# Kernel tuning notes

Measured on AMD Instinct MI355X. Metric: run time of the kernel, lower is better.

## Reference

```python
import jax, jax.numpy as jnp
import numpy as np

B, L, D, O = 16, 128, 256, 256

def setup_inputs() -> dict:
    key = jax.random.key(0)
    k1, k2, k3, k4, k5 = jax.random.split(key, 5)
    text = jax.random.normal(k1, (B, L, D), dtype=jnp.float32)
    adj = jax.random.uniform(k2, (B, L, L), dtype=jnp.float32)
    dep_embed = jax.random.normal(k3, (B, L, L, D), dtype=jnp.float32)
    weight = jax.random.normal(k4, (D, O), dtype=jnp.float32) * (1.0 / np.sqrt(D))
    bias = jax.random.normal(k5, (O,), dtype=jnp.float32) * 0.01
    return {"text": text, "adj": adj, "dep_embed": dep_embed, "weight": weight, "bias": bias}

def reference(text, adj, dep_embed, weight, bias):
    # val_sum[b,j,i,d] = text[b,j,d] + dep_embed[b,j,i,d]
    val_sum = text[:, :, None, :] + dep_embed            # [B,L,L,D]
    hidden = val_sum @ weight                            # [B,L,L,O]
    # torch: output[b,i,o] = sum_j adj[b,i,j] * hidden[b,j,i,o]
    out = jnp.einsum('bij,bjio->bio', adj, hidden)       # [B,L,O]
    out = out + bias
    return jax.nn.relu(out)
```

## Files before the change

### kernel.cpp

```cpp
#include <hip/hip_runtime.h>


constexpr int Bc = 16, Lc = 128, Dc = 256, Oc = 256;
constexpr int ITILE = 4;

__global__ __launch_bounds__(256)
void gc_fused(const float4* __restrict__ text4,
              const float*  __restrict__ adj,
              const float4* __restrict__ dep4,
              const float4* __restrict__ weight4,
              const float4* __restrict__ bias4,
              float4* __restrict__ out4)
{
    const int b  = blockIdx.x >> 5;
    const int i0 = (blockIdx.x & 31) * ITILE;
    const int t  = threadIdx.x;
    const int ig = t >> 6;
    const int dg = t & 63;

    __shared__ float s_adj[ITILE][Lc];
    __shared__ float s_S[ITILE][Dc];

    for (int k = t; k < ITILE * Lc; k += 256) {
        int row = k >> 7;
        int col = k & (Lc - 1);
        s_adj[row][col] = adj[((b * Lc) + i0 + row) * Lc + col];
    }
    __syncthreads();

    const int i = i0 + ig;

    float4 acc = {0.f, 0.f, 0.f, 0.f};
    const float4* tb = text4 + (size_t)b * Lc * (Dc / 4) + dg;
    const float4* db = dep4  + ((size_t)b * Lc * Lc + (size_t)i) * (Dc / 4) + dg;
    #pragma unroll 4
    for (int j = 0; j < Lc; ++j) {
        float  a  = s_adj[ig][j];
        float4 tx = tb[(size_t)j * (Dc / 4)];
        float4 de = db[(size_t)j * Lc * (Dc / 4)];
        acc.x = fmaf(a, tx.x + de.x, acc.x);
        acc.y = fmaf(a, tx.y + de.y, acc.y);
        acc.z = fmaf(a, tx.z + de.z, acc.z);
        acc.w = fmaf(a, tx.w + de.w, acc.w);
    }
    ((float4*)&s_S[ig][0])[dg] = acc;
    __syncthreads();

    float4 oacc = bias4[dg];
    #pragma unroll 4
    for (int d = 0; d < Dc; ++d) {
        float  s = s_S[ig][d];
        float4 w = weight4[d * (Oc / 4) + dg];
        oacc.x = fmaf(s, w.x, oacc.x);
        oacc.y = fmaf(s, w.y, oacc.y);
        oacc.z = fmaf(s, w.z, oacc.z);
        oacc.w = fmaf(s, w.w, oacc.w);
    }
    oacc.x = fmaxf(oacc.x, 0.f);
    oacc.y = fmaxf(oacc.y, 0.f);
    oacc.z = fmaxf(oacc.z, 0.f);
    oacc.w = fmaxf(oacc.w, 0.f);
    out4[((size_t)b * Lc + i) * (Oc / 4) + dg] = oacc;
}

extern "C" void kernel_launch(void* const* d_in, const int* in_sizes, int n_in,
                              void* d_out, int out_size, void* d_ws, size_t ws_size,
                              hipStream_t stream) {
    const float4* text4   = (const float4*)d_in[0];
    const float*  adj     = (const float*) d_in[1];
    const float4* dep4    = (const float4*)d_in[2];
    const float4* weight4 = (const float4*)d_in[3];
    const float4* bias4   = (const float4*)d_in[4];
    float4*       out4    = (float4*)d_out;

    dim3 grid(Bc * (Lc / ITILE));
    dim3 block(256);
    gc_fused<<<grid, block, 0, stream>>>(text4, adj, dep4, weight4, bias4, out4);
}
```

Baseline: 389.6 us.

## Split j-reduction and weight GEMV across warps with one row per block

Each block now handles a single output row i instead of four, with the four wavefronts splitting the j range of the adjacency-weighted sum and the d range of the weight projection, then reducing partials in shared memory. This quadruples the grid to 2048 blocks and shortens each thread's serial dependency chain, aiming to expose more memory-level parallelism on the dominant dep_embed stream. It adds two extra barriers and shared-memory reductions, and the block no longer reuses weight loads across four rows. A launch-bounds occupancy hint is also added.

```diff
diff --git a/kernel.cpp b/kernel.cpp
--- a/kernel.cpp
+++ b/kernel.cpp
@@ -2,9 +2,8 @@
 
 
 constexpr int Bc = 16, Lc = 128, Dc = 256, Oc = 256;
-constexpr int ITILE = 4;
 
-__global__ __launch_bounds__(256)
+__global__ __launch_bounds__(256, 8)
 void gc_fused(const float4* __restrict__ text4,
               const float*  __restrict__ adj,
               const float4* __restrict__ dep4,
@@ -12,55 +11,68 @@
               const float4* __restrict__ bias4,
               float4* __restrict__ out4)
 {
-    const int b  = blockIdx.x >> 5;
-    const int i0 = (blockIdx.x & 31) * ITILE;
-    const int t  = threadIdx.x;
-    const int ig = t >> 6;
-    const int dg = t & 63;
+    const int b    = blockIdx.x >> 7;
+    const int i    = blockIdx.x & 127;
+    const int t    = threadIdx.x;
+    const int w    = t >> 6;
+    const int lane = t & 63;
 
-    __shared__ float s_adj[ITILE][Lc];
-    __shared__ float s_S[ITILE][Dc];
+    __shared__ float s_adj[Lc];
+    __shared__ float s_part[4][Dc];
+    __shared__ float s_S[Dc];
+    __shared__ float s_po[4][Oc];
 
-    for (int k = t; k < ITILE * Lc; k += 256) {
-        int row = k >> 7;
-        int col = k & (Lc - 1);
-        s_adj[row][col] = adj[((b * Lc) + i0 + row) * Lc + col];
-    }
+    if (t < Lc) s_adj[t] = adj[((size_t)b * Lc + i) * Lc + t];
     __syncthreads();
 
-    const int i = i0 + ig;
-
     float4 acc = {0.f, 0.f, 0.f, 0.f};
-    const float4* tb = text4 + (size_t)b * Lc * (Dc / 4) + dg;
-    const float4* db = dep4  + ((size_t)b * Lc * Lc + (size_t)i) * (Dc / 4) + dg;
+    const int j0 = w * 32;
+    const float4* tb = text4 + (size_t)b * Lc * (Dc / 4) + lane;
+    const float4* db = dep4  + ((size_t)b * Lc * Lc + (size_t)i) * (Dc / 4) + lane;
     #pragma unroll 4
-    for (int j = 0; j < Lc; ++j) {
-        float  a  = s_adj[ig][j];
+    for (int jj = 0; jj < 32; ++jj) {
+        const int j = j0 + jj;
+        float  a  = s_adj[j];
         float4 tx = tb[(size_t)j * (Dc / 4)];
-        float4 de = db[(size_t)j * Lc * (Dc / 4)];
+        float4 de = db[(size_t)j * (size_t)Lc * (Dc / 4)];
         acc.x = fmaf(a, tx.x + de.x, acc.x);
         acc.y = fmaf(a, tx.y + de.y, acc.y);
         acc.z = fmaf(a, tx.z + de.z, acc.z);
         acc.w = fmaf(a, tx.w + de.w, acc.w);
     }
-    ((float4*)&s_S[ig][0])[dg] = acc;
+    ((float4*)&s_part[w][0])[lane] = acc;
     __syncthreads();
 
-    float4 oacc = bias4[dg];
-    #pragma unroll 4
-    for (int d = 0; d < Dc; ++d) {
-        float  s = s_S[ig][d];
-        float4 w = weight4[d * (Oc / 4) + dg];
-        oacc.x = fmaf(s, w.x, oacc.x);
-        oacc.y = fmaf(s, w.y, oacc.y);
-        oacc.z = fmaf(s, w.z, oacc.z);
-        oacc.w = fmaf(s, w.w, oacc.w);
+    s_S[t] = s_part[0][t] + s_part[1][t] + s_part[2][t] + s_part[3][t];
+    __syncthreads();
+
+    float4 oacc = {0.f, 0.f, 0.f, 0.f};
+    #pragma unroll 8
+    for (int k = 0; k < 64; ++k) {
+        const int d = w * 64 + k;
+        float  s  = s_S[d];
+        float4 wv = weight4[d * (Oc / 4) + lane];
+        oacc.x = fmaf(s, wv.x, oacc.x);
+        oacc.y = fmaf(s, wv.y, oacc.y);
+        oacc.z = fmaf(s, wv.z, oacc.z);
+        oacc.w = fmaf(s, wv.w, oacc.w);
     }
-    oacc.x = fmaxf(oacc.x, 0.f);
-    oacc.y = fmaxf(oacc.y, 0.f);
-    oacc.z = fmaxf(oacc.z, 0.f);
-    oacc.w = fmaxf(oacc.w, 0.f);
-    out4[((size_t)b * Lc + i) * (Oc / 4) + dg] = oacc;
+    ((float4*)&s_po[w][0])[lane] = oacc;
+    __syncthreads();
+
+    if (w == 0) {
+        float4 r = bias4[lane];
+        #pragma unroll
+        for (int p = 0; p < 4; ++p) {
+            float4 v = ((float4*)&s_po[p][0])[lane];
+            r.x += v.x; r.y += v.y; r.z += v.z; r.w += v.w;
+        }
+        r.x = fmaxf(r.x, 0.f);
+        r.y = fmaxf(r.y, 0.f);
+        r.z = fmaxf(r.z, 0.f);
+        r.w = fmaxf(r.w, 0.f);
+        out4[((size_t)b * Lc + i) * (Oc / 4) + lane] = r;
+    }
 }
 
 extern "C" void kernel_launch(void* const* d_in, const int* in_sizes, int n_in,
@@ -73,7 +85,7 @@
     const float4* bias4   = (const float4*)d_in[4];
     float4*       out4    = (float4*)d_out;
 
-    dim3 grid(Bc * (Lc / ITILE));
+    dim3 grid(Bc * Lc);
     dim3 block(256);
     gc_fused<<<grid, block, 0, stream>>>(text4, adj, dep4, weight4, bias4, out4);
 }
```

New measurement: 377.3 us. 3.2% less time.
